# Kernel tuning notes

Measured on AMD Instinct MI355X. Metric: run time of the kernel, lower is better.

The kernel has to match this reference:

```python
import jax, jax.numpy as jnp
import numpy as np

N_HEADS = 32
EPS = 1e-7
ROPE_BASE = 10000.0


def rms_norm(x, gamma):
    return x / jnp.sqrt(EPS + jnp.mean(x * x, axis=-1, keepdims=True)) * gamma


def rope_tables(seq_len, head_dim, dtype=jnp.float32):
    inv_freq = 1.0 / (ROPE_BASE ** (jnp.arange(0, head_dim, 2, dtype=jnp.float32) / head_dim))
    angles = jnp.arange(seq_len, dtype=jnp.float32)[:, None] * inv_freq[None, :]  # [S, D/2]
    angles = jnp.concatenate([angles, angles], axis=-1)  # [S, D]
    return jnp.cos(angles).astype(dtype), jnp.sin(angles).astype(dtype)


def apply_rope(x, cos, sin):
    # x: [B, H, S, D]; cos/sin: [S, D]
    d = x.shape[-1]
    x1, x2 = x[..., : d // 2], x[..., d // 2 :]
    rotated = jnp.concatenate([-x2, x1], axis=-1)
    return x * cos[None, None] + rotated * sin[None, None]


def setup_inputs() -> dict:
    key = jax.random.key(0)
    ks = jax.random.split(key, 9)
    B, S, D, Hd = 1, 2048, 4096, 11008
    s = lambda k, shape, fan: jax.random.normal(k, shape, jnp.float32) * (fan ** -0.5)
    return {
        "X": jax.random.normal(ks[0], (B, S, D), jnp.float32),
        "Wq": s(ks[1], (D, D), D),
        "Wk": s(ks[2], (D, D), D),
        "Wv": s(ks[3], (D, D), D),
        "Wo": s(ks[4], (D, D), D),
        "bo": jnp.zeros((D,), jnp.float32),
        "gamma1": jnp.ones((D,), jnp.float32),
        "gamma2": jnp.ones((D,), jnp.float32),
        "W1": s(ks[5], (D, Hd), D),
        "W2": s(ks[6], (D, Hd), D),
        "W3": s(ks[7], (Hd, D), Hd),
    }


def reference(X, Wq, Wk, Wv, Wo, bo, gamma1, gamma2, W1, W2, W3):
    B, S, D = X.shape
    H = N_HEADS
    hd = D // H

    # --- attention sublayer ---
    h = rms_norm(X, gamma1)
    q = (h @ Wq).reshape(B, S, H, hd).transpose(0, 2, 1, 3)  # [B,H,S,hd]
    k = (h @ Wk).reshape(B, S, H, hd).transpose(0, 2, 1, 3)
    v = (h @ Wv).reshape(B, S, H, hd).transpose(0, 2, 1, 3)

    cos, sin = rope_tables(S, hd, X.dtype)
    q = apply_rope(q, cos, sin)
    k = apply_rope(k, cos, sin)

    scores = jnp.einsum("bhsd,bhtd->bhst", q, k) / jnp.sqrt(jnp.asarray(hd, X.dtype))
    causal = jnp.tril(jnp.ones((S, S), bool))
    scores = jnp.where(causal, scores, -jnp.inf)
    attn = jax.nn.softmax(scores, axis=-1)
    out = jnp.einsum("bhst,bhtd->bhsd", attn, v)
    out = out.transpose(0, 2, 1, 3).reshape(B, S, D)
    out = out @ Wo + bo
    X = X + out

    # --- SwiGLU FFN sublayer ---
    h2 = rms_norm(X, gamma2)
    x1 = h2 @ W1
    x2 = h2 @ W2
    ff = (x1 * jax.nn.sigmoid(x1) * x2) @ W3
    return X + ff
```

## Files before the change

kernel.cpp:

```cpp
#include <hip/hip_runtime.h>
#include <hip/hip_bf16.h>
#include <cstdint>
#include <cmath>

typedef __bf16 bf16;
typedef __attribute__((ext_vector_type(8))) __bf16 bf16x8;
typedef __attribute__((ext_vector_type(4))) __bf16 bf16x4;
typedef __attribute__((ext_vector_type(4))) float f32x4;

__device__ __forceinline__ void gload_lds16(const void* g, void* l) {
  __builtin_amdgcn_global_load_lds((__attribute__((address_space(1))) void*)g,
                                   (__attribute__((address_space(3))) void*)l,
                                   16, 0, 0);
}

template<int BM, int EPI>
__global__ __launch_bounds__(512, 2) void gemmd(
    const bf16* __restrict__ A, const bf16* __restrict__ Bt, void* __restrict__ Cv,
    const float* __restrict__ bias, const float* __restrict__ resid,
    const float* __restrict__ cosT, const float* __restrict__ sinT,
    bf16* __restrict__ q_out, bf16* __restrict__ k_out, bf16* __restrict__ v_out,
    int M, int N, int K, int gm) {
  extern __shared__ char lds[];
  constexpr int ASZ = BM * 128;
  constexpr int BUFS = ASZ + 32768;
  constexpr int MF = BM / 64;
  constexpr int LA = BM / 64;

  const int tid = threadIdx.x;
  const int wave = tid >> 6, lane = tid & 63;
  const int wr = wave >> 1, wc = wave & 1;
  const int l15 = lane & 15, l4 = lane >> 4;
  const int qq = gridDim.x >> 3;
  const int wgid = (blockIdx.x & 7) * qq + (blockIdx.x >> 3);
  const int tm = wgid % gm, tn = wgid / gm;
  const long brow = (long)tm * BM, bcol = (long)tn * 256;
  const int NT = K >> 6;
  const bf16* Ab = A + brow * K;
  const bf16* Bb = Bt + bcol * K;

  f32x4 acc[MF][8];
  #pragma unroll
  for (int i = 0; i < MF; ++i)
    #pragma unroll
    for (int j = 0; j < 8; ++j) acc[i][j] = (f32x4){0.f, 0.f, 0.f, 0.f};

  bf16x8 a[MF], b[8];

  auto stage = [&](int T) {
    const long kofs = (long)T << 6;
    char* wb = lds + (T & 1) * BUFS;
    #pragma unroll
    for (int i = 0; i < LA; ++i) {
      const int slot = i * 512 + tid, r = slot >> 3, c0 = slot & 7;
      gload_lds16(Ab + (long)r * K + kofs + ((c0 ^ (r & 7)) << 3), wb + slot * 16);
    }
    #pragma unroll
    for (int i = 0; i < 4; ++i) {
      const int slot = i * 512 + tid, r = slot >> 3, c0 = slot & 7;
      gload_lds16(Bb + (long)r * K + kofs + ((c0 ^ (r & 7)) << 3), wb + ASZ + slot * 16);
    }
  };

  stage(0);
  __syncthreads();

  for (int g = 0; g < NT; ++g) {
    const int pg = (g & 1) * BUFS;
    if (g + 1 < NT) stage(g + 1);
    #pragma unroll
    for (int ks = 0; ks < 2; ++ks) {
      #pragma unroll
      for (int nf = 0; nf < 8; ++nf) {
        const int r = wc * 128 + nf * 16 + l15;
        b[nf] = *(const bf16x8*)(lds + pg + ASZ + r * 128 + (((ks * 4 + l4) ^ (r & 7)) << 4));
      }
      #pragma unroll
      for (int mf = 0; mf < MF; ++mf) {
        const int r = wr * (BM / 4) + mf * 16 + l15;
        a[mf] = *(const bf16x8*)(lds + pg + r * 128 + (((ks * 4 + l4) ^ (r & 7)) << 4));
      }
      #pragma unroll
      for (int mf = 0; mf < MF; ++mf)
        #pragma unroll
        for (int nf = 0; nf < 8; ++nf)
          acc[mf][nf] = __builtin_amdgcn_mfma_f32_16x16x32_bf16(
              a[mf], b[nf], acc[mf][nf], 0, 0, 0);
    }
    __syncthreads();
  }

  if (EPI == 1 || EPI == 2) {
    #pragma unroll
    for (int mf = 0; mf < MF; ++mf) {
      const long row0 = brow + wr * (BM / 4) + mf * 16 + l4 * 4;
      #pragma unroll
      for (int nf = 0; nf < 8; ++nf) {
        const long col = bcol + wc * 128 + nf * 16 + l15;
        #pragma unroll
        for (int rj = 0; rj < 4; ++rj) {
          const long idx = (row0 + rj) * N + col;
          const float v = acc[mf][nf][rj];
          if (EPI == 1) ((float*)Cv)[idx] = v + bias[col] + resid[idx];
          else          ((float*)Cv)[idx] = v + resid[idx];
        }
      }
    }
  } else if (EPI == 3) {
    const int region = (int)(bcol >> 12);
    const int hc = (int)(bcol & 4095) + wc * 128;
    const int h = hc >> 7;
    if (region < 2) {
      bf16* dh = (region == 0 ? q_out : k_out) + (long)h * 2048 * 128;
      #pragma unroll
      for (int mf = 0; mf < MF; ++mf) {
        #pragma unroll
        for (int rj = 0; rj < 4; ++rj) {
          const int s = (int)brow + wr * (BM / 4) + mf * 16 + l4 * 4 + rj;
          const float* cr = cosT + s * 64;
          const float* sr = sinT + s * 64;
          #pragma unroll
          for (int nfp = 0; nfp < 4; ++nfp) {
            const int d = nfp * 16 + l15;
            const float c = cr[d], sn = sr[d];
            const float x1 = acc[mf][nfp][rj], x2 = acc[mf][nfp + 4][rj];
            dh[(long)s * 128 + d]      = (bf16)(x1 * c - x2 * sn);
            dh[(long)s * 128 + d + 64] = (bf16)(x2 * c + x1 * sn);
          }
        }
      }
    } else {
      bf16* dh = v_out + (long)h * 128 * 2048;
      #pragma unroll
      for (int mf = 0; mf < MF; ++mf) {
        const int s0 = (int)brow + wr * (BM / 4) + mf * 16 + l4 * 4;
        #pragma unroll
        for (int nf = 0; nf < 8; ++nf) {
          const int d = nf * 16 + l15;
          bf16x4 v;
          #pragma unroll
          for (int rj = 0; rj < 4; ++rj) v[rj] = (bf16)acc[mf][nf][rj];
          *(bf16x4*)(dh + (long)d * 2048 + s0) = v;
        }
      }
    }
  } else if (EPI == 4) {
    #pragma unroll
    for (int mf = 0; mf < MF; ++mf) {
      #pragma unroll
      for (int rj = 0; rj < 4; ++rj) {
        const int s = (int)brow + wr * (BM / 4) + mf * 16 + l4 * 4 + rj;
        bf16* gr = (bf16*)Cv + (long)s * 11008;
        #pragma unroll
        for (int nfp = 0; nfp < 4; ++nfp) {
          const int col = (int)bcol + wc * 128 + nfp * 32 + l15;
          const int jj = ((col >> 5) << 4) + l15;
          const float x1 = acc[mf][2 * nfp][rj], x2 = acc[mf][2 * nfp + 1][rj];
          const float sg = x1 / (1.f + __expf(-x1));
          gr[jj] = (bf16)(sg * x2);
        }
      }
    }
  }
}

__device__ __forceinline__ void trans64(
    const float* __restrict__ in, bf16* __restrict__ out,
    int R, int C, int bx, int by, int ilv, int off) {
  __shared__ float t[64][65];
  const int lr = threadIdx.x >> 4;
  const int lc4 = (threadIdx.x & 15) * 4;
  #pragma unroll
  for (int i = 0; i < 4; ++i) {
    const int r = lr + i * 16;
    const float4 v = *(const float4*)(in + (long)(by * 64 + r) * C + bx * 64 + lc4);
    t[r][lc4] = v.x; t[r][lc4 + 1] = v.y; t[r][lc4 + 2] = v.z; t[r][lc4 + 3] = v.w;
  }
  __syncthreads();
  const int oc = threadIdx.x >> 4;
  const int or4 = (threadIdx.x & 15) * 4;
  #pragma unroll
  for (int i = 0; i < 4; ++i) {
    const int c = oc + i * 16;
    const int j = bx * 64 + c;
    const int rdst = ilv ? (((j >> 4) << 5) + off + (j & 15)) : j;
    bf16x4 v;
    #pragma unroll
    for (int k = 0; k < 4; ++k) v[k] = (bf16)t[or4 + k][c];
    *(bf16x4*)(out + (long)rdst * R + by * 64 + or4) = v;
  }
}

__global__ __launch_bounds__(256) void prep_kernel(
    const float* __restrict__ Wq, const float* __restrict__ Wk,
    const float* __restrict__ Wv, const float* __restrict__ Wo,
    const float* __restrict__ W1, const float* __restrict__ W2,
    const float* __restrict__ W3,
    bf16* __restrict__ WqkvT, bf16* __restrict__ WoT,
    bf16* __restrict__ W12T, bf16* __restrict__ W3T,
    float* __restrict__ cosT, float* __restrict__ sinT) {
  const int bid = blockIdx.x;
  if (bid < 16384) {
    const int seg = bid >> 12, idx = bid & 4095;
    const float* in = (seg == 0 ? Wq : seg == 1 ? Wk : seg == 2 ? Wv : Wo);
    bf16* out = (seg == 3 ? WoT : WqkvT + (long)seg * 4096 * 4096);
    trans64(in, out, 4096, 4096, idx & 63, idx >> 6, 0, 0);
  } else if (bid < 38400) {
    const int idx = bid - 16384;
    const int seg = idx / 11008, li = idx % 11008;
    trans64(seg ? W2 : W1, W12T, 4096, 11008, li % 172, li / 172, 1, seg * 16);
  } else if (bid < 49408) {
    const int idx = bid - 38400;
    trans64(W3, W3T, 11008, 4096, idx & 63, idx >> 6, 0, 0);
  } else {
    const int gidx = (bid - 49408) * 256 + threadIdx.x;
    const int i = gidx & 63, s = gidx >> 6;
    const float inv = powf(10000.f, -(float)i / 64.f);
    const float ang = (float)s * inv;
    cosT[gidx] = cosf(ang);
    sinT[gidx] = sinf(ang);
  }
}

__global__ __launch_bounds__(256) void rmsnorm_kernel(
    const float* __restrict__ X, const float* __restrict__ gamma,
    bf16* __restrict__ out, int D) {
  const int row = blockIdx.x;
  const float* xr = X + (long)row * D;
  float ss = 0.f;
  for (int i = threadIdx.x * 4; i < D; i += 1024) {
    float4 v = *(const float4*)(xr + i);
    ss += v.x * v.x + v.y * v.y + v.z * v.z + v.w * v.w;
  }
  #pragma unroll
  for (int off = 32; off; off >>= 1) ss += __shfl_down(ss, off, 64);
  __shared__ float wsum[4];
  if ((threadIdx.x & 63) == 0) wsum[threadIdx.x >> 6] = ss;
  __syncthreads();
  const float tot = wsum[0] + wsum[1] + wsum[2] + wsum[3];
  const float scale = rsqrtf(1e-7f + tot / (float)D);
  bf16* orow = out + (long)row * D;
  for (int i = threadIdx.x * 4; i < D; i += 1024) {
    float4 v = *(const float4*)(xr + i);
    float4 g = *(const float4*)(gamma + i);
    orow[i]     = (bf16)(v.x * scale * g.x);
    orow[i + 1] = (bf16)(v.y * scale * g.y);
    orow[i + 2] = (bf16)(v.z * scale * g.z);
    orow[i + 3] = (bf16)(v.w * scale * g.w);
  }
}

__global__ __launch_bounds__(256) void attn_kernel(
    const bf16* __restrict__ qh, const bf16* __restrict__ kh,
    const bf16* __restrict__ vt, bf16* __restrict__ outb) {
  constexpr int S = 2048;
  const int qb = blockIdx.x, head = blockIdx.y;
  const int tid = threadIdx.x, wave = tid >> 6, lane = tid & 63;
  __shared__ bf16 Ks[2][64 * 128];
  __shared__ bf16 Vs[2][128 * 64];
  __shared__ bf16 Plds[4][16 * 64];
  const bf16* qhh = qh + (long)head * S * 128;
  const bf16* khh = kh + (long)head * S * 128;
  const bf16* vth = vt + (long)head * 128 * S;

  const int l15 = lane & 15, l4 = lane >> 4;
  const int qrow = qb * 64 + wave * 16 + l15;
  bf16x8 qf[4];
  #pragma unroll
  for (int kf = 0; kf < 4; ++kf)
    qf[kf] = *(const bf16x8*)(qhh + (long)qrow * 128 + kf * 32 + l4 * 8);

  auto stageKV = [&](int tb, int buf) {
    #pragma unroll
    for (int i = 0; i < 4; ++i) {
      const int c = wave + 4 * i;
      const int krlow = (c & 3) * 4 + l4;
      gload_lds16(khh + (long)(tb * 64 + c * 4 + l4) * 128 + ((l15 ^ krlow) * 8),
                  Ks[buf] + c * 512);
      gload_lds16(vth + (long)(c * 8 + (lane >> 3)) * S + tb * 64 +
                      (((lane & 7) ^ (lane >> 3)) * 8),
                  Vs[buf] + c * 512);
    }
  };

  float m_r[4], l_r[4];
  #pragma unroll
  for (int r = 0; r < 4; ++r) { m_r[r] = -INFINITY; l_r[r] = 0.f; }
  f32x4 oacc[8] = {};
  const float scale = 0.08838834764831845f;

  stageKV(0, 0);
  __syncthreads();

  for (int tb = 0; tb <= qb; ++tb) {
    const int buf = tb & 1;
    if (tb < qb) stageKV(tb + 1, buf ^ 1);

    f32x4 sf[4];
    #pragma unroll
    for (int ft = 0; ft < 4; ++ft) {
      f32x4 acn = {};
      #pragma unroll
      for (int kf = 0; kf < 4; ++kf) {
        bf16x8 kfr = *(const bf16x8*)(Ks[buf] + (ft * 16 + l15) * 128 +
                                      (((kf * 4 + l4) ^ l15) * 8));
        acn = __builtin_amdgcn_mfma_f32_16x16x32_bf16(qf[kf], kfr, acn, 0, 0, 0);
      }
      #pragma unroll
      for (int r = 0; r < 4; ++r) sf[ft][r] = acn[r] * scale;
    }
    if (tb == qb) {
      #pragma unroll
      for (int ft = 0; ft < 4; ++ft) {
        const int t_l = ft * 16 + l15;
        #pragma unroll
        for (int r = 0; r < 4; ++r)
          if (t_l > wave * 16 + l4 * 4 + r) sf[ft][r] = -INFINITY;
      }
    }
    float scl[4];
    #pragma unroll
    for (int r = 0; r < 4; ++r) {
      float mx = fmaxf(fmaxf(sf[0][r], sf[1][r]), fmaxf(sf[2][r], sf[3][r]));
      mx = fmaxf(mx, __shfl_xor(mx, 1, 64));
      mx = fmaxf(mx, __shfl_xor(mx, 2, 64));
      mx = fmaxf(mx, __shfl_xor(mx, 4, 64));
      mx = fmaxf(mx, __shfl_xor(mx, 8, 64));
      const float mnew = fmaxf(m_r[r], mx);
      scl[r] = __expf(m_r[r] - mnew);
      m_r[r] = mnew;
      float rs = 0.f;
      #pragma unroll
      for (int ft = 0; ft < 4; ++ft) {
        const float pexp = __expf(sf[ft][r] - mnew);
        sf[ft][r] = pexp;
        rs += pexp;
      }
      rs += __shfl_xor(rs, 1, 64);
      rs += __shfl_xor(rs, 2, 64);
      rs += __shfl_xor(rs, 4, 64);
      rs += __shfl_xor(rs, 8, 64);
      l_r[r] = l_r[r] * scl[r] + rs;
    }
    #pragma unroll
    for (int ft = 0; ft < 4; ++ft)
      #pragma unroll
      for (int r = 0; r < 4; ++r) {
        const int q = l4 * 4 + r;
        const int sl = (ft * 2 + (l15 >> 3)) ^ (q & 7);
        Plds[wave][q * 64 + sl * 8 + (l15 & 7)] = (bf16)sf[ft][r];
      }
    #pragma unroll
    for (int fd = 0; fd < 8; ++fd)
      #pragma unroll
      for (int r = 0; r < 4; ++r) oacc[fd][r] *= scl[r];
    #pragma unroll
    for (int fd = 0; fd < 8; ++fd) {
      #pragma unroll
      for (int kt = 0; kt < 2; ++kt) {
        bf16x8 pa = *(const bf16x8*)(&Plds[wave][l15 * 64 +
                        (((kt * 4 + l4) ^ (l15 & 7)) * 8)]);
        bf16x8 vb = *(const bf16x8*)(Vs[buf] + (fd * 16 + l15) * 64 +
                        (((kt * 4 + l4) ^ (l15 & 7)) * 8));
        oacc[fd] = __builtin_amdgcn_mfma_f32_16x16x32_bf16(pa, vb, oacc[fd], 0, 0, 0);
      }
    }
    __syncthreads();
  }
  #pragma unroll
  for (int fd = 0; fd < 8; ++fd) {
    #pragma unroll
    for (int r = 0; r < 4; ++r) {
      const long row = qb * 64 + wave * 16 + l4 * 4 + r;
      outb[row * 4096 + head * 128 + fd * 16 + l15] = (bf16)(oacc[fd][r] / l_r[r]);
    }
  }
}

extern "C" void kernel_launch(void* const* d_in, const int* in_sizes, int n_in,
                              void* d_out, int out_size, void* d_ws, size_t ws_size,
                              hipStream_t stream) {
  const float* X  = (const float*)d_in[0];
  const float* Wq = (const float*)d_in[1];
  const float* Wk = (const float*)d_in[2];
  const float* Wv = (const float*)d_in[3];
  const float* Wo = (const float*)d_in[4];
  const float* bo = (const float*)d_in[5];
  const float* g1 = (const float*)d_in[6];
  const float* g2 = (const float*)d_in[7];
  const float* W1 = (const float*)d_in[8];
  const float* W2 = (const float*)d_in[9];
  const float* W3 = (const float*)d_in[10];
  float* out = (float*)d_out;

  hipFuncSetAttribute((const void*)gemmd<256, 3>, hipFuncAttributeMaxDynamicSharedMemorySize, 131072);
  hipFuncSetAttribute((const void*)gemmd<256, 4>, hipFuncAttributeMaxDynamicSharedMemorySize, 131072);
  hipFuncSetAttribute((const void*)gemmd<128, 1>, hipFuncAttributeMaxDynamicSharedMemorySize, 98304);
  hipFuncSetAttribute((const void*)gemmd<128, 2>, hipFuncAttributeMaxDynamicSharedMemorySize, 98304);

  char* p = (char*)d_ws;
  auto alloc = [&](size_t bytes) {
    char* r = p;
    p += (bytes + 255) & ~(size_t)255;
    return r;
  };
  float* cosT = (float*)alloc(2048 * 64 * 4);
  float* sinT = (float*)alloc(2048 * 64 * 4);
  bf16* WqkvT = (bf16*)alloc(12288L * 4096 * 2);
  bf16* WoT  = (bf16*)alloc(4096L * 4096 * 2);
  bf16* W12T = (bf16*)alloc(22016L * 4096 * 2);
  bf16* W3T  = (bf16*)alloc(4096L * 11008 * 2);
  bf16* qhB  = (bf16*)alloc(2048L * 4096 * 2);
  bf16* khB  = (bf16*)alloc(2048L * 4096 * 2);
  bf16* vtB  = (bf16*)alloc(2048L * 4096 * 2);
  bf16* hbuf = (bf16*)alloc(2048L * 4096 * 2);
  bf16* h2   = (bf16*)alloc(2048L * 4096 * 2);
  float* X2  = (float*)alloc(2048L * 4096 * 4);

  bf16* gsw = (bf16*)WqkvT;
  bf16* attnb = hbuf;

  prep_kernel<<<49920, 256, 0, stream>>>(Wq, Wk, Wv, Wo, W1, W2, W3,
                                         WqkvT, WoT, W12T, W3T, cosT, sinT);

  rmsnorm_kernel<<<2048, 256, 0, stream>>>(X, g1, hbuf, 4096);

  gemmd<256, 3><<<384, 512, 131072, stream>>>(hbuf, WqkvT, nullptr, nullptr, nullptr,
                                              cosT, sinT, qhB, khB, vtB,
                                              2048, 12288, 4096, 8);

  attn_kernel<<<dim3(32, 32), 256, 0, stream>>>(qhB, khB, vtB, attnb);

  gemmd<128, 1><<<256, 512, 98304, stream>>>(attnb, WoT, X2, bo, X,
                                             nullptr, nullptr, nullptr, nullptr, nullptr,
                                             2048, 4096, 4096, 16);

  rmsnorm_kernel<<<2048, 256, 0, stream>>>(X2, g2, h2, 4096);

  gemmd<256, 4><<<688, 512, 131072, stream>>>(h2, W12T, gsw, nullptr, nullptr,
                                              nullptr, nullptr, nullptr, nullptr, nullptr,
                                              2048, 22016, 4096, 8);

  gemmd<128, 2><<<256, 512, 98304, stream>>>(gsw, W3T, out, nullptr, X2,
                                             nullptr, nullptr, nullptr, nullptr, nullptr,
                                             2048, 4096, 11008, 16);
}
```

Measured before the change: 1.307 ms.

## Split-K the down-projection GEMM with 256-row tiles and a bf16 combine pass

The final W3 GEMM (K=11008) switches from 128-row tiles with a fused residual epilogue to 256-row tiles split into two K halves. Each half writes bf16 partials into reused q/k buffers, and a new combine kernel adds the two partials plus the residual in fp32. The main loop also now loads both k-substeps of A and B fragments from LDS before issuing the MFMAs. The aim is better per-block reuse with the larger tile while keeping 256 workgroups, at the cost of an extra elementwise pass, extra partial traffic, and bf16 rounding of the partial sums.

Result: faster. 1.221 ms (-6.6%).

```diff
diff --git a/kernel.cpp b/kernel.cpp
--- a/kernel.cpp
+++ b/kernel.cpp
@@ -20,7 +20,7 @@
     const float* __restrict__ bias, const float* __restrict__ resid,
     const float* __restrict__ cosT, const float* __restrict__ sinT,
     bf16* __restrict__ q_out, bf16* __restrict__ k_out, bf16* __restrict__ v_out,
-    int M, int N, int K, int gm) {
+    int M, int N, int K, int ksd, int gm) {
   extern __shared__ char lds[];
   constexpr int ASZ = BM * 128;
   constexpr int BUFS = ASZ + 32768;
@@ -33,11 +33,16 @@
   const int l15 = lane & 15, l4 = lane >> 4;
   const int qq = gridDim.x >> 3;
   const int wgid = (blockIdx.x & 7) * qq + (blockIdx.x >> 3);
-  const int tm = wgid % gm, tn = wgid / gm;
+  const int tm = wgid % gm;
+  int tq = wgid / gm;
+  int split = 0;
+  if (EPI == 5) { split = tq / (N >> 8); tq = tq % (N >> 8); }
+  const int tn = tq;
   const long brow = (long)tm * BM, bcol = (long)tn * 256;
+  const long koff = (long)split * K;
   const int NT = K >> 6;
-  const bf16* Ab = A + brow * K;
-  const bf16* Bb = Bt + bcol * K;
+  const bf16* Ab = A + brow * ksd + koff;
+  const bf16* Bb = Bt + bcol * ksd + koff;
 
   f32x4 acc[MF][8];
   #pragma unroll
@@ -45,7 +50,7 @@
     #pragma unroll
     for (int j = 0; j < 8; ++j) acc[i][j] = (f32x4){0.f, 0.f, 0.f, 0.f};
 
-  bf16x8 a[MF], b[8];
+  bf16x8 a[MF][2], b[8][2];
 
   auto stage = [&](int T) {
     const long kofs = (long)T << 6;
@@ -53,12 +58,12 @@
     #pragma unroll
     for (int i = 0; i < LA; ++i) {
       const int slot = i * 512 + tid, r = slot >> 3, c0 = slot & 7;
-      gload_lds16(Ab + (long)r * K + kofs + ((c0 ^ (r & 7)) << 3), wb + slot * 16);
+      gload_lds16(Ab + (long)r * ksd + kofs + ((c0 ^ (r & 7)) << 3), wb + slot * 16);
     }
     #pragma unroll
     for (int i = 0; i < 4; ++i) {
       const int slot = i * 512 + tid, r = slot >> 3, c0 = slot & 7;
-      gload_lds16(Bb + (long)r * K + kofs + ((c0 ^ (r & 7)) << 3), wb + ASZ + slot * 16);
+      gload_lds16(Bb + (long)r * ksd + kofs + ((c0 ^ (r & 7)) << 3), wb + ASZ + slot * 16);
     }
   };
 
@@ -69,28 +74,31 @@
     const int pg = (g & 1) * BUFS;
     if (g + 1 < NT) stage(g + 1);
     #pragma unroll
-    for (int ks = 0; ks < 2; ++ks) {
-      #pragma unroll
-      for (int nf = 0; nf < 8; ++nf) {
+    for (int nf = 0; nf < 8; ++nf)
+      #pragma unroll
+      for (int ks = 0; ks < 2; ++ks) {
         const int r = wc * 128 + nf * 16 + l15;
-        b[nf] = *(const bf16x8*)(lds + pg + ASZ + r * 128 + (((ks * 4 + l4) ^ (r & 7)) << 4));
-      }
-      #pragma unroll
-      for (int mf = 0; mf < MF; ++mf) {
+        b[nf][ks] = *(const bf16x8*)(lds + pg + ASZ + r * 128 + (((ks * 4 + l4) ^ (r & 7)) << 4));
+      }
+    #pragma unroll
+    for (int mf = 0; mf < MF; ++mf)
+      #pragma unroll
+      for (int ks = 0; ks < 2; ++ks) {
         const int r = wr * (BM / 4) + mf * 16 + l15;
-        a[mf] = *(const bf16x8*)(lds + pg + r * 128 + (((ks * 4 + l4) ^ (r & 7)) << 4));
-      }
+        a[mf][ks] = *(const bf16x8*)(lds + pg + r * 128 + (((ks * 4 + l4) ^ (r & 7)) << 4));
+      }
+    #pragma unroll
+    for (int ks = 0; ks < 2; ++ks)
       #pragma unroll
       for (int mf = 0; mf < MF; ++mf)
         #pragma unroll
         for (int nf = 0; nf < 8; ++nf)
           acc[mf][nf] = __builtin_amdgcn_mfma_f32_16x16x32_bf16(
-              a[mf], b[nf], acc[mf][nf], 0, 0, 0);
-    }
+              a[mf][ks], b[nf][ks], acc[mf][nf], 0, 0, 0);
     __syncthreads();
   }
 
-  if (EPI == 1 || EPI == 2) {
+  if (EPI == 1) {
     #pragma unroll
     for (int mf = 0; mf < MF; ++mf) {
       const long row0 = brow + wr * (BM / 4) + mf * 16 + l4 * 4;
@@ -100,10 +108,21 @@
         #pragma unroll
         for (int rj = 0; rj < 4; ++rj) {
           const long idx = (row0 + rj) * N + col;
-          const float v = acc[mf][nf][rj];
-          if (EPI == 1) ((float*)Cv)[idx] = v + bias[col] + resid[idx];
-          else          ((float*)Cv)[idx] = v + resid[idx];
+          ((float*)Cv)[idx] = acc[mf][nf][rj] + bias[col] + resid[idx];
         }
+      }
+    }
+  } else if (EPI == 5) {
+    bf16* dst = (split == 0 ? q_out : v_out);
+    #pragma unroll
+    for (int mf = 0; mf < MF; ++mf) {
+      const long row0 = brow + wr * (BM / 4) + mf * 16 + l4 * 4;
+      #pragma unroll
+      for (int nf = 0; nf < 8; ++nf) {
+        const long col = bcol + wc * 128 + nf * 16 + l15;
+        #pragma unroll
+        for (int rj = 0; rj < 4; ++rj)
+          dst[(row0 + rj) * N + col] = (bf16)acc[mf][nf][rj];
       }
     }
   } else if (EPI == 3) {
@@ -162,6 +181,17 @@
       }
     }
   }
+}
+
+__global__ __launch_bounds__(256) void combine_kernel(
+    const bf16* __restrict__ p0, const bf16* __restrict__ p1,
+    const float* __restrict__ X2, float* __restrict__ out) {
+  const long i = ((long)blockIdx.x * 256 + threadIdx.x) * 8;
+  bf16x8 a = *(const bf16x8*)(p0 + i);
+  bf16x8 b = *(const bf16x8*)(p1 + i);
+  #pragma unroll
+  for (int j = 0; j < 8; ++j)
+    out[i + j] = (float)a[j] + (float)b[j] + X2[i + j];
 }
 
 __device__ __forceinline__ void trans64(
@@ -395,8 +425,8 @@
 
   hipFuncSetAttribute((const void*)gemmd<256, 3>, hipFuncAttributeMaxDynamicSharedMemorySize, 131072);
   hipFuncSetAttribute((const void*)gemmd<256, 4>, hipFuncAttributeMaxDynamicSharedMemorySize, 131072);
+  hipFuncSetAttribute((const void*)gemmd<256, 5>, hipFuncAttributeMaxDynamicSharedMemorySize, 131072);
   hipFuncSetAttribute((const void*)gemmd<128, 1>, hipFuncAttributeMaxDynamicSharedMemorySize, 98304);
-  hipFuncSetAttribute((const void*)gemmd<128, 2>, hipFuncAttributeMaxDynamicSharedMemorySize, 98304);
 
   char* p = (char*)d_ws;
   auto alloc = [&](size_t bytes) {
@@ -419,6 +449,8 @@
 
   bf16* gsw = (bf16*)WqkvT;
   bf16* attnb = hbuf;
+  bf16* P0 = qhB;
+  bf16* P1 = khB;
 
   prep_kernel<<<49920, 256, 0, stream>>>(Wq, Wk, Wv, Wo, W1, W2, W3,
                                          WqkvT, WoT, W12T, W3T, cosT, sinT);
@@ -427,21 +459,23 @@
 
   gemmd<256, 3><<<384, 512, 131072, stream>>>(hbuf, WqkvT, nullptr, nullptr, nullptr,
                                               cosT, sinT, qhB, khB, vtB,
-                                              2048, 12288, 4096, 8);
+                                              2048, 12288, 4096, 4096, 8);
 
   attn_kernel<<<dim3(32, 32), 256, 0, stream>>>(qhB, khB, vtB, attnb);
 
   gemmd<128, 1><<<256, 512, 98304, stream>>>(attnb, WoT, X2, bo, X,
                                              nullptr, nullptr, nullptr, nullptr, nullptr,
-                                             2048, 4096, 4096, 16);
+                                             2048, 4096, 4096, 4096, 16);
 
   rmsnorm_kernel<<<2048, 256, 0, stream>>>(X2, g2, h2, 4096);
 
   gemmd<256, 4><<<688, 512, 131072, stream>>>(h2, W12T, gsw, nullptr, nullptr,
                                               nullptr, nullptr, nullptr, nullptr, nullptr,
-                                              2048, 22016, 4096, 8);
-
-  gemmd<128, 2><<<256, 512, 98304, stream>>>(gsw, W3T, out, nullptr, X2,
-                                             nullptr, nullptr, nullptr, nullptr, nullptr,
-                                             2048, 4096, 11008, 16);
-}
+                                              2048, 22016, 4096, 4096, 8);
+
+  gemmd<256, 5><<<256, 512, 131072, stream>>>(gsw, W3T, nullptr, nullptr, nullptr,
+                                              nullptr, nullptr, P0, nullptr, P1,
+                                              2048, 4096, 5504, 11008, 8);
+
+  combine_kernel<<<4096, 256, 0, stream>>>(P0, P1, X2, out);
+}
```
